# Performance work log

Measured on AMD Instinct MI355X. Metric: run time of the kernel, lower is better.

## Reference

```python
import jax, jax.numpy as jnp
import numpy as np

B, N, T, H = 128, 64, 1000, 16
TAU, VTH, EPS = 2.0, 0.5, 1e-5

# Heaviside spike with ATan surrogate gradient (alpha=2.0)
@jax.custom_vjp
def spike(u):
    return (u > 0).astype(u.dtype)

def _spike_fwd(u):
    return (u > 0).astype(u.dtype), u

def _spike_bwd(u, g):
    return (g / (1.0 + (2.0 * u) ** 2),)

spike.defvjp(_spike_fwd, _spike_bwd)


def setup_inputs() -> dict:
    key = jax.random.key(0)
    ks = jax.random.split(key, 6)
    x = jax.random.normal(ks[0], (B, 1, N, T), dtype=jnp.float32)
    # 1x1 Conv1d on a single input channel == per-output-channel scale + bias
    q_w = jax.random.normal(ks[1], (H,), dtype=jnp.float32) * 0.5
    q_b = jnp.zeros((H,), jnp.float32)
    k_w = jax.random.normal(ks[2], (H,), dtype=jnp.float32) * 0.5
    k_b = jnp.zeros((H,), jnp.float32)
    conv_w = jax.random.normal(ks[3], (H, 1, 1, 15), dtype=jnp.float32) * 0.1
    conv_b = jnp.zeros((H,), jnp.float32)
    bn_gamma = jnp.ones((H,), jnp.float32)
    bn_beta = jnp.zeros((H,), jnp.float32)
    fc_w = jax.random.normal(ks[4], (4, H * N), dtype=jnp.float32) * 0.02
    fc_b = jnp.zeros((4,), jnp.float32)
    return dict(x=x, q_w=q_w, q_b=q_b, k_w=k_w, k_b=k_b, conv_w=conv_w,
                conv_b=conv_b, bn_gamma=bn_gamma, bn_beta=bn_beta,
                fc_w=fc_w, fc_b=fc_b)


def reference(x, q_w, q_b, k_w, k_b, conv_w, conv_b, bn_gamma, bn_beta, fc_w, fc_b):
    xs = x[:, 0]                                    # [B, N, T]
    # Dynamic graph attention on per-channel variance "energy"
    energy = jnp.var(xs, axis=-1, ddof=1)           # [B, N] (torch unbiased var)
    Q = energy[:, None, :] * q_w[None, :, None] + q_b[None, :, None]  # [B,H,N]
    K = energy[:, None, :] * k_w[None, :, None] + k_b[None, :, None]
    attn = jnp.einsum('bhi,bhj->bij', Q, K) * (H ** -0.5)             # [B,N,N]
    attn = jnp.where(jnp.eye(N, dtype=bool)[None], -1e9, attn)
    w = jax.nn.softmax(attn, axis=-1)
    z_gcn = jnp.einsum('bij,bjt->bit', w, xs)[:, None] + x            # [B,1,N,T]
    # ANN spatial block: Conv2d(1,16,(1,15),pad=(0,7)) + BN (batch stats) + ELU
    z = jax.lax.conv_general_dilated(
        z_gcn, conv_w, window_strides=(1, 1), padding=((0, 0), (7, 7)),
        dimension_numbers=('NCHW', 'OIHW', 'NCHW')) + conv_b[None, :, None, None]
    mu = jnp.mean(z, axis=(0, 2, 3), keepdims=True)
    var = jnp.var(z, axis=(0, 2, 3), keepdims=True)
    z = (z - mu) * jax.lax.rsqrt(var + EPS)
    z = z * bn_gamma[None, :, None, None] + bn_beta[None, :, None, None]
    z = jax.nn.elu(z)                               # [B,H,N,T]
    # LIF temporal scan
    def step(v, xt):
        v = v * (1.0 - 1.0 / TAU) + xt
        s = spike(v - VTH)
        return v - s * VTH, s
    xt_seq = jnp.moveaxis(z, -1, 0)                 # [T,B,H,N]
    _, spikes = jax.lax.scan(step, jnp.zeros(z.shape[:-1], z.dtype), xt_seq)
    firing_rate = jnp.mean(spikes, axis=0)          # [B,H,N]
    z_feat = firing_rate.reshape(firing_rate.shape[0], -1)  # [B, H*N]
    logits = z_feat @ fc_w.T + fc_b                 # [B,4] (dropout = eval identity)
    return logits, z_feat, w
```

## Files before the change

kernel.cpp:

```cpp
#include <hip/hip_runtime.h>

#define B_ 128
#define N_ 64
#define T_ 1000
#define H_ 16

typedef float v2f __attribute__((ext_vector_type(2)));

__device__ __forceinline__ v2f mkv2(float a, float b) { v2f t; t.x = a; t.y = b; return t; }

__global__ __launch_bounds__(256) void k_energy(const float* __restrict__ x, float* __restrict__ energy) {
    int row = blockIdx.x;
    const float* xr = x + (size_t)row * T_;
    float s = 0.f, s2 = 0.f;
    for (int t4 = threadIdx.x; t4 < 250; t4 += 256) {
        float4 v = ((const float4*)xr)[t4];
        s += v.x + v.y + v.z + v.w;
        s2 += v.x*v.x + v.y*v.y + v.z*v.z + v.w*v.w;
    }
    __shared__ float r1[256], r2[256];
    r1[threadIdx.x] = s; r2[threadIdx.x] = s2;
    __syncthreads();
    for (int off = 128; off > 0; off >>= 1) {
        if (threadIdx.x < off) {
            r1[threadIdx.x] += r1[threadIdx.x + off];
            r2[threadIdx.x] += r2[threadIdx.x + off];
        }
        __syncthreads();
    }
    if (threadIdx.x == 0) {
        float S = r1[0], S2 = r2[0];
        energy[row] = (S2 - S * S / (float)T_) / (float)(T_ - 1);
    }
}

#define ZTC 128
__global__ __launch_bounds__(256) void k_zgcn(const float* __restrict__ energy,
        const float* __restrict__ q_w, const float* __restrict__ q_b,
        const float* __restrict__ k_w, const float* __restrict__ k_b,
        const float* __restrict__ x, float* __restrict__ zg,
        float* __restrict__ wmat_out, double* __restrict__ stats) {
    int b = blockIdx.y;
    int t0 = blockIdx.x * ZTC;
    int tid = threadIdx.x;
    if (blockIdx.x == 0 && b == 0 && tid < 163) stats[tid] = 0.0;
    __shared__ __attribute__((aligned(16))) float wsh[64 * 64];
    __shared__ __attribute__((aligned(16))) float xs[64][ZTC];
    __shared__ float en[64];
    float (*red1)[4] = (float(*)[4])&xs[0][0];
    float (*red2)[4] = (float(*)[4])&xs[2][0];
    if (tid < 64) en[tid] = energy[b * 64 + tid];
    __syncthreads();
    float alpha = 0.f, beta = 0.f;
    #pragma unroll
    for (int hh = 0; hh < H_; ++hh) {
        alpha = fmaf(q_w[hh], k_w[hh], alpha);
        beta  = fmaf(q_b[hh], k_w[hh], beta);
    }
    int row = tid >> 2, q = tid & 3;
    float si = 0.25f * fmaf(alpha, en[row], beta);
    float vals[16];
    float m = -3.0e38f;
    #pragma unroll
    for (int k = 0; k < 16; ++k) {
        int j = q * 16 + k;
        float a = si * en[j];
        if (j == row) a = -3.0e38f;
        vals[k] = a;
        m = fmaxf(m, a);
    }
    red1[row][q] = m;
    __syncthreads();
    float m4 = fmaxf(fmaxf(red1[row][0], red1[row][1]), fmaxf(red1[row][2], red1[row][3]));
    float sum = 0.f;
    #pragma unroll
    for (int k = 0; k < 16; ++k) {
        float p = __expf(vals[k] - m4);
        vals[k] = p;
        sum += p;
    }
    red2[row][q] = sum;
    __syncthreads();
    float den = red2[row][0] + red2[row][1] + red2[row][2] + red2[row][3];
    float inv = 1.f / den;
    #pragma unroll
    for (int k = 0; k < 16; ++k) vals[k] *= inv;
    __syncthreads();
    #pragma unroll
    for (int k = 0; k < 16; ++k) wsh[row * 64 + q * 16 + k] = vals[k];
    if (blockIdx.x == 0) {
        float* wr = wmat_out + (size_t)b * 4096 + row * 64 + q * 16;
        ((float4*)wr)[0] = float4{vals[0],  vals[1],  vals[2],  vals[3]};
        ((float4*)wr)[1] = float4{vals[4],  vals[5],  vals[6],  vals[7]};
        ((float4*)wr)[2] = float4{vals[8],  vals[9],  vals[10], vals[11]};
        ((float4*)wr)[3] = float4{vals[12], vals[13], vals[14], vals[15]};
    }
    const float* xb = x + (size_t)b * 64 * T_;
    for (int i = tid; i < 2048; i += 256) {
        int jj = i >> 5;
        int c4 = i & 31;
        int tt = t0 + c4 * 4;
        float4 val;
        if (tt + 3 < T_) val = *(const float4*)(xb + jj * T_ + tt);
        else {
            val.x = (tt     < T_) ? xb[jj * T_ + tt]     : 0.f;
            val.y = (tt + 1 < T_) ? xb[jj * T_ + tt + 1] : 0.f;
            val.z = (tt + 2 < T_) ? xb[jj * T_ + tt + 2] : 0.f;
            val.w = (tt + 3 < T_) ? xb[jj * T_ + tt + 3] : 0.f;
        }
        *(float4*)&xs[jj][c4 * 4] = val;
    }
    __syncthreads();
    int gi = tid >> 5, gt = tid & 31;
    int ii0 = gi * 8, tt0 = gt * 4;
    float4 acc[8];
    #pragma unroll
    for (int r = 0; r < 8; ++r) acc[r] = float4{0.f, 0.f, 0.f, 0.f};
    for (int jj = 0; jj < 64; ++jj) {
        float4 xv = *(const float4*)&xs[jj][tt0];
        #pragma unroll
        for (int r = 0; r < 8; ++r) {
            float wv = wsh[(ii0 + r) * 64 + jj];
            acc[r].x += wv * xv.x; acc[r].y += wv * xv.y;
            acc[r].z += wv * xv.z; acc[r].w += wv * xv.w;
        }
    }
    int tt = t0 + tt0;
    #pragma unroll
    for (int r = 0; r < 8; ++r) {
        float4 res = *(const float4*)&xs[ii0 + r][tt0];
        acc[r].x += res.x; acc[r].y += res.y; acc[r].z += res.z; acc[r].w += res.w;
        float* dst = zg + (size_t)b * 64 * T_ + (size_t)(ii0 + r) * T_;
        if (tt + 3 < T_) {
            *(float4*)(dst + tt) = acc[r];
        } else {
            if (tt     < T_) dst[tt]     = acc[r].x;
            if (tt + 1 < T_) dst[tt + 1] = acc[r].y;
            if (tt + 2 < T_) dst[tt + 2] = acc[r].z;
            if (tt + 3 < T_) dst[tt + 3] = acc[r].w;
        }
    }
}

__global__ __launch_bounds__(256) void k_autocorr(const float* __restrict__ zg, double* __restrict__ stats) {
    __shared__ float rows[8][1070];
    int row0 = blockIdx.x * 8;
    for (int idx = threadIdx.x; idx < 8 * 1070; idx += 256) {
        int rr = idx / 1070, j = idx - rr * 1070;
        rows[rr][j] = (j < T_) ? zg[(size_t)(row0 + rr) * T_ + j] : 0.f;
    }
    __syncthreads();
    int r = threadIdx.x >> 5, q = threadIdx.x & 31;
    const float* p = &rows[r][0];
    int t = q * 33;
    float w0=p[t+0], w1=p[t+1], w2=p[t+2], w3=p[t+3], w4=p[t+4], w5=p[t+5], w6=p[t+6],
          w7=p[t+7], w8=p[t+8], w9=p[t+9], w10=p[t+10], w11=p[t+11], w12=p[t+12], w13=p[t+13], w14;
    float a0=0.f,a1=0.f,a2=0.f,a3=0.f,a4=0.f,a5=0.f,a6=0.f,a7=0.f,a8=0.f,a9=0.f,
          a10=0.f,a11=0.f,a12=0.f,a13=0.f,a14=0.f, s1=0.f;
    #define ASTEP(wA,wB,wC,wD,wE,wF,wG,wH,wI,wJ,wK,wL,wM,wN,wO, off) { \
        wO = p[t + (off) + 14]; \
        s1 += wA; \
        a0  = fmaf(wA,wA,a0);  a1  = fmaf(wA,wB,a1);  a2  = fmaf(wA,wC,a2);  \
        a3  = fmaf(wA,wD,a3);  a4  = fmaf(wA,wE,a4);  a5  = fmaf(wA,wF,a5);  \
        a6  = fmaf(wA,wG,a6);  a7  = fmaf(wA,wH,a7);  a8  = fmaf(wA,wI,a8);  \
        a9  = fmaf(wA,wJ,a9);  a10 = fmaf(wA,wK,a10); a11 = fmaf(wA,wL,a11); \
        a12 = fmaf(wA,wM,a12); a13 = fmaf(wA,wN,a13); a14 = fmaf(wA,wO,a14); }
    #define AR0(o)  ASTEP(w0,w1,w2,w3,w4,w5,w6,w7,w8,w9,w10,w11,w12,w13,w14, o)
    #define AR1(o)  ASTEP(w1,w2,w3,w4,w5,w6,w7,w8,w9,w10,w11,w12,w13,w14,w0, o)
    #define AR2(o)  ASTEP(w2,w3,w4,w5,w6,w7,w8,w9,w10,w11,w12,w13,w14,w0,w1, o)
    #define AR3(o)  ASTEP(w3,w4,w5,w6,w7,w8,w9,w10,w11,w12,w13,w14,w0,w1,w2, o)
    #define AR4(o)  ASTEP(w4,w5,w6,w7,w8,w9,w10,w11,w12,w13,w14,w0,w1,w2,w3, o)
    #define AR5(o)  ASTEP(w5,w6,w7,w8,w9,w10,w11,w12,w13,w14,w0,w1,w2,w3,w4, o)
    #define AR6(o)  ASTEP(w6,w7,w8,w9,w10,w11,w12,w13,w14,w0,w1,w2,w3,w4,w5, o)
    #define AR7(o)  ASTEP(w7,w8,w9,w10,w11,w12,w13,w14,w0,w1,w2,w3,w4,w5,w6, o)
    #define AR8(o)  ASTEP(w8,w9,w10,w11,w12,w13,w14,w0,w1,w2,w3,w4,w5,w6,w7, o)
    #define AR9(o)  ASTEP(w9,w10,w11,w12,w13,w14,w0,w1,w2,w3,w4,w5,w6,w7,w8, o)
    #define AR10(o) ASTEP(w10,w11,w12,w13,w14,w0,w1,w2,w3,w4,w5,w6,w7,w8,w9, o)
    #define AR11(o) ASTEP(w11,w12,w13,w14,w0,w1,w2,w3,w4,w5,w6,w7,w8,w9,w10, o)
    #define AR12(o) ASTEP(w12,w13,w14,w0,w1,w2,w3,w4,w5,w6,w7,w8,w9,w10,w11, o)
    #define AR13(o) ASTEP(w13,w14,w0,w1,w2,w3,w4,w5,w6,w7,w8,w9,w10,w11,w12, o)
    #define AR14(o) ASTEP(w14,w0,w1,w2,w3,w4,w5,w6,w7,w8,w9,w10,w11,w12,w13, o)
    for (int mi = 0; mi < 2; ++mi) {
        AR0(0) AR1(1) AR2(2) AR3(3) AR4(4) AR5(5) AR6(6) AR7(7)
        AR8(8) AR9(9) AR10(10) AR11(11) AR12(12) AR13(13) AR14(14)
        t += 15;
    }
    AR0(0) AR1(1) AR2(2)
    #undef ASTEP
    __syncthreads();
    float eacc = 0.f;
    int v = threadIdx.x;
    if (v < 147) {
        int mode, ia, ib;
        if (v < 105) { mode = 0; ia = v / 15; ib = ia + (v % 15); }
        else if (v < 133) {
            int idx = v - 105; int i = 0, len = 7;
            while (idx >= len) { idx -= len; ++i; --len; }
            mode = 2; ia = 993 + i; ib = 993 + i + idx;
        }
        else if (v < 140) { mode = 1; ia = 0; ib = v - 133; }
        else { mode = 1; ia = 993 + (v - 140); ib = 999; }
        for (int rr = 0; rr < 8; ++rr) {
            const float* zr = &rows[rr][0];
            float val;
            if (mode != 1) val = zr[ia] * zr[ib];
            else { val = 0.f; for (int i = ia; i <= ib; ++i) val += zr[i]; }
            eacc += val;
        }
    }
    __syncthreads();
    float* red = &rows[0][0];
    int tid = threadIdx.x;
    red[tid*17+0]=a0;  red[tid*17+1]=a1;  red[tid*17+2]=a2;  red[tid*17+3]=a3;
    red[tid*17+4]=a4;  red[tid*17+5]=a5;  red[tid*17+6]=a6;  red[tid*17+7]=a7;
    red[tid*17+8]=a8;  red[tid*17+9]=a9;  red[tid*17+10]=a10; red[tid*17+11]=a11;
    red[tid*17+12]=a12; red[tid*17+13]=a13; red[tid*17+14]=a14; red[tid*17+15]=s1;
    __syncthreads();
    for (int off = 128; off > 0; off >>= 1) {
        if (tid < off)
            for (int k = 0; k < 16; ++k) red[tid*17+k] += red[(tid+off)*17+k];
        __syncthreads();
    }
    if (tid < 16) atomicAdd(&stats[tid], (double)red[tid]);
    if (v < 147) atomicAdd(&stats[16 + v], (double)eacc);
}

__global__ __launch_bounds__(256, 2) void k_scan(const float* __restrict__ zg,
        const double* __restrict__ stats, const float* __restrict__ conv_w,
        const float* __restrict__ gamma, const float* __restrict__ beta,
        float* __restrict__ zfeat) {
    int tid = threadIdx.x;
    int h = tid & 15, r = tid >> 4;
    int row0 = blockIdx.x * 16;
    __shared__ float scsh_s[256];
    if (tid < 16) {
        int hh = tid;
        const double M = (double)(B_ * N_) * (double)T_;
        double w[15];
        #pragma unroll
        for (int k = 0; k < 15; ++k) w[k] = (double)conv_w[hh * 15 + k];
        double SA = stats[15];
        const double* HP  = stats + 16;
        const double* TP  = stats + 16 + 105;
        const double* PRE = stats + 16 + 133;
        const double* SUF = stats + 16 + 140;
        double so = 0.0;
        #pragma unroll
        for (int k = 0; k < 15; ++k) {
            double U = SA;
            if (k < 7)      U -= SUF[k];
            else if (k > 7) U -= PRE[k - 8];
            so += w[k] * U;
        }
        double mean_o = so / M;
        double q = 0.0;
        #pragma unroll
        for (int k = 0; k < 15; ++k)
        #pragma unroll
        for (int k2 = 0; k2 < 15; ++k2) {
            int a = (k < k2) ? k : k2;
            int d = (k < k2) ? (k2 - k) : (k - k2);
            double G = stats[d];
            if (a >= 8)
                for (int i = 0; i <= a - 8; ++i) G -= HP[i * 15 + d];
            if (a + d <= 6)
                for (int i = a + 993; i <= 999 - d; ++i) {
                    int ip = i - 993;
                    G -= TP[ip * 7 - ip * (ip - 1) / 2 + d];
                }
            q += w[k] * w[k2] * G;
        }
        double var = q / M - mean_o * mean_o;
        double sc = (double)gamma[hh] / sqrt(var + 1e-5);
        scsh_s[240 + hh] = (float)((double)beta[hh] - mean_o * sc);
        #pragma unroll
        for (int k = 0; k < 15; ++k) scsh_s[hh * 15 + k] = (float)(w[k] * sc);
    }
    __syncthreads();
    float c0 = scsh_s[h*15+0],  c1 = scsh_s[h*15+1],  c2 = scsh_s[h*15+2],  c3 = scsh_s[h*15+3];
    float c4 = scsh_s[h*15+4],  c5 = scsh_s[h*15+5],  c6 = scsh_s[h*15+6],  c7 = scsh_s[h*15+7];
    float c8 = scsh_s[h*15+8],  c9 = scsh_s[h*15+9],  c10 = scsh_s[h*15+10], c11 = scsh_s[h*15+11];
    float c12 = scsh_s[h*15+12], c13 = scsh_s[h*15+13], c14 = scsh_s[h*15+14];
    float sh = scsh_s[240 + h];
    v2f d0 = {c0,c0},  d1 = {c1,c1},  d2 = {c2,c2},  d3 = {c3,c3},  d4 = {c4,c4};
    v2f d5 = {c5,c5},  d6 = {c6,c6},  d7 = {c7,c7},  d8 = {c8,c8},  d9 = {c9,c9};
    v2f d10 = {c10,c10}, d11 = {c11,c11}, d12 = {c12,c12}, d13 = {c13,c13}, d14 = {c14,c14};
    v2f shp2 = {sh, sh}, zr2 = {0.f, 0.f};
    const float* zrow = zg + (size_t)(row0 + r) * T_;
    float u = 2.f, cnt = 0.f;
    float4 g[17];
    const float4 f4z = {0.f, 0.f, 0.f, 0.f};

    #define PKF(acc, c, xp)  asm("v_pk_fma_f32 %0, %1, %2, %0" : "+v"(acc) : "v"(c), "v"(xp))
    #define PKADD(dd, aa, bb) asm("v_pk_add_f32 %0, %1, %2" : "=v"(dd) : "v"(aa), "v"(bb))

    #define PL(n) ( (((n)&3)==0) ? mkv2(g[(n)>>2].x, g[(n)>>2].y) \
                  : (((n)&3)==1) ? mkv2(g[(n)>>2].y, g[(n)>>2].z) \
                  : (((n)&3)==2) ? mkv2(g[(n)>>2].z, g[(n)>>2].w) \
                  :                mkv2(g[(n)>>2].w, g[((n)>>2)+1].x) )

    #define PAIRM(m) { \
        v2f vA = shp2, vB = zr2; \
        PKF(vA, d0,  PL(2*(m)+1));  PKF(vB, d1,  PL(2*(m)+2)); \
        PKF(vA, d2,  PL(2*(m)+3));  PKF(vB, d3,  PL(2*(m)+4)); \
        PKF(vA, d4,  PL(2*(m)+5));  PKF(vB, d5,  PL(2*(m)+6)); \
        PKF(vA, d6,  PL(2*(m)+7));  PKF(vB, d7,  PL(2*(m)+8)); \
        PKF(vA, d8,  PL(2*(m)+9));  PKF(vB, d9,  PL(2*(m)+10)); \
        PKF(vA, d10, PL(2*(m)+11)); PKF(vB, d11, PL(2*(m)+12)); \
        PKF(vA, d12, PL(2*(m)+13)); PKF(vB, d13, PL(2*(m)+14)); \
        PKF(vA, d14, PL(2*(m)+15)); \
        v2f vz; PKADD(vz, vA, vB); \
        float ex_ = __expf(fminf(vz.x, 0.f)); \
        float ey_ = __expf(fminf(vz.y, 0.f)); \
        float px_ = fmaxf(vz.x, 0.f) + ex_; \
        float py_ = fmaxf(vz.y, 0.f) + ey_; \
        u = fmaf(0.5f, u, px_); \
        float s0_ = (u > 2.5f) ? 1.f : 0.f; cnt += s0_; u = fmaf(-0.5f, s0_, u); \
        u = fmaf(0.5f, u, py_); \
        float s1_ = (u > 2.5f) ? 1.f : 0.f; cnt += s1_; u = fmaf(-0.5f, s1_, u); }

    #define PAIRS24 \
        PAIRM(0)  PAIRM(1)  PAIRM(2)  PAIRM(3)  PAIRM(4)  PAIRM(5) \
        PAIRM(6)  PAIRM(7)  PAIRM(8)  PAIRM(9)  PAIRM(10) PAIRM(11) \
        PAIRM(12) PAIRM(13) PAIRM(14) PAIRM(15) PAIRM(16) PAIRM(17) \
        PAIRM(18) PAIRM(19) PAIRM(20) PAIRM(21) PAIRM(22) PAIRM(23)

    #define PAIRS20 \
        PAIRM(0)  PAIRM(1)  PAIRM(2)  PAIRM(3)  PAIRM(4)  PAIRM(5) \
        PAIRM(6)  PAIRM(7)  PAIRM(8)  PAIRM(9)  PAIRM(10) PAIRM(11) \
        PAIRM(12) PAIRM(13) PAIRM(14) PAIRM(15) PAIRM(16) PAIRM(17) \
        PAIRM(18) PAIRM(19)

    {
        g[0] = f4z; g[1] = f4z;
        #pragma unroll
        for (int i = 2; i < 16; ++i) g[i] = *(const float4*)(zrow + 4*i - 8);
        PAIRS24
    }
    #pragma unroll 1
    for (int c = 1; c < 20; ++c) {
        const float* pc = zrow + 48*c - 8;
        #pragma unroll
        for (int i = 0; i < 16; ++i) g[i] = *(const float4*)(pc + 4*i);
        PAIRS24
    }
    {
        const float* pc = zrow + 952;
        #pragma unroll
        for (int i = 0; i < 12; ++i) g[i] = *(const float4*)(pc + 4*i);
        g[12] = f4z; g[13] = f4z; g[14] = f4z; g[15] = f4z;
        PAIRS20
    }
    #undef PKF
    #undef PKADD
    #undef PL
    #undef PAIRM
    #undef PAIRS24
    #undef PAIRS20
    int row = row0 + r;
    int b = row >> 6, i = row & 63;
    zfeat[(size_t)b * 1024 + h * 64 + i] = cnt * (1.0f / (float)T_);
}

__global__ __launch_bounds__(256) void k_fc(const float* __restrict__ zfeat, const float* __restrict__ fc_w,
                     const float* __restrict__ fc_b, float* __restrict__ logits) {
    int b = blockIdx.x;
    const float* zf = zfeat + (size_t)b * 1024;
    float a0 = 0.f, a1 = 0.f, a2 = 0.f, a3 = 0.f;
    for (int f = threadIdx.x; f < 1024; f += 256) {
        float z = zf[f];
        a0 += z * fc_w[f];
        a1 += z * fc_w[1024 + f];
        a2 += z * fc_w[2048 + f];
        a3 += z * fc_w[3072 + f];
    }
    __shared__ float red[4][256];
    red[0][threadIdx.x] = a0; red[1][threadIdx.x] = a1;
    red[2][threadIdx.x] = a2; red[3][threadIdx.x] = a3;
    __syncthreads();
    for (int off = 128; off > 0; off >>= 1) {
        if (threadIdx.x < off) {
            red[0][threadIdx.x] += red[0][threadIdx.x + off];
            red[1][threadIdx.x] += red[1][threadIdx.x + off];
            red[2][threadIdx.x] += red[2][threadIdx.x + off];
            red[3][threadIdx.x] += red[3][threadIdx.x + off];
        }
        __syncthreads();
    }
    if (threadIdx.x < 4) logits[b * 4 + threadIdx.x] = red[threadIdx.x][0] + fc_b[threadIdx.x];
}

extern "C" void kernel_launch(void* const* d_in, const int* in_sizes, int n_in,
                              void* d_out, int out_size, void* d_ws, size_t ws_size,
                              hipStream_t stream) {
    (void)in_sizes; (void)n_in; (void)out_size; (void)ws_size;
    const float* x      = (const float*)d_in[0];
    const float* q_w    = (const float*)d_in[1];
    const float* q_b    = (const float*)d_in[2];
    const float* k_w    = (const float*)d_in[3];
    const float* k_b    = (const float*)d_in[4];
    const float* conv_w = (const float*)d_in[5];
    const float* bn_g   = (const float*)d_in[7];
    const float* bn_b   = (const float*)d_in[8];
    const float* fc_w   = (const float*)d_in[9];
    const float* fc_b   = (const float*)d_in[10];

    float* out    = (float*)d_out;
    float* logits = out;
    float* zfeat  = out + 512;
    float* wmat   = out + 512 + 131072;

    char* ws      = (char*)d_ws;
    float* energy = (float*)ws;
    float* zg     = (float*)(ws + 32768);
    double* stats = (double*)(ws + 32768 + 32768000);

    k_energy<<<B_ * N_, 256, 0, stream>>>(x, energy);
    k_zgcn<<<dim3(8, B_), 256, 0, stream>>>(energy, q_w, q_b, k_w, k_b, x, zg, wmat, stats);
    k_autocorr<<<B_ * N_ / 8, 256, 0, stream>>>(zg, stats);
    k_scan<<<B_ * N_ / 16, 256, 0, stream>>>(zg, stats, conv_w, bn_g, bn_b, zfeat);
    k_fc<<<B_, 256, 0, stream>>>(zfeat, fc_w, fc_b, logits);
}
```

Baseline: 182.9 us.

## Stage scan input rows through double-buffered LDS with shifted copies for pair loads

The LIF scan kernel used to have each thread load its own overlapping float4 windows of its input row from global memory, so all 16 threads sharing a row loaded the same data. It now loads each 48-sample chunk of 16 rows cooperatively into a double-buffered LDS tile, plus a second copy shifted by one element so odd-offset pairs can be read as aligned 8-byte loads. The next chunk is prefetched into registers while the current one is computed, and a rotating register window reuses the pairs across steps. This cuts redundant global traffic and register pressure, and drops the occupancy hint from launch bounds, at the cost of LDS traffic and a barrier per chunk.

```diff
diff --git a/kernel.cpp b/kernel.cpp
--- a/kernel.cpp
+++ b/kernel.cpp
@@ -6,8 +6,6 @@
 #define H_ 16
 
 typedef float v2f __attribute__((ext_vector_type(2)));
-
-__device__ __forceinline__ v2f mkv2(float a, float b) { v2f t; t.x = a; t.y = b; return t; }
 
 __global__ __launch_bounds__(256) void k_energy(const float* __restrict__ x, float* __restrict__ energy) {
     int row = blockIdx.x;
@@ -225,14 +223,16 @@
     if (v < 147) atomicAdd(&stats[16 + v], (double)eacc);
 }
 
-__global__ __launch_bounds__(256, 2) void k_scan(const float* __restrict__ zg,
+__global__ __launch_bounds__(256) void k_scan(const float* __restrict__ zg,
         const double* __restrict__ stats, const float* __restrict__ conv_w,
         const float* __restrict__ gamma, const float* __restrict__ beta,
         float* __restrict__ zfeat) {
+    __shared__ float in_s[2][16][68];
+    __shared__ float in2[2][16][70];
+    __shared__ float scsh_s[256];
     int tid = threadIdx.x;
     int h = tid & 15, r = tid >> 4;
     int row0 = blockIdx.x * 16;
-    __shared__ float scsh_s[256];
     if (tid < 16) {
         int hh = tid;
         const double M = (double)(B_ * N_) * (double)T_;
@@ -286,77 +286,115 @@
     v2f d5 = {c5,c5},  d6 = {c6,c6},  d7 = {c7,c7},  d8 = {c8,c8},  d9 = {c9,c9};
     v2f d10 = {c10,c10}, d11 = {c11,c11}, d12 = {c12,c12}, d13 = {c13,c13}, d14 = {c14,c14};
     v2f shp2 = {sh, sh}, zr2 = {0.f, 0.f};
-    const float* zrow = zg + (size_t)(row0 + r) * T_;
     float u = 2.f, cnt = 0.f;
-    float4 g[17];
-    const float4 f4z = {0.f, 0.f, 0.f, 0.f};
-
-    #define PKF(acc, c, xp)  asm("v_pk_fma_f32 %0, %1, %2, %0" : "+v"(acc) : "v"(c), "v"(xp))
+    float ld0, ld1, ld2, ld3;
+    int su = tid & 63, sr = tid >> 6;
+
+    #define STAGE_LOAD(cc) { \
+        int g = (cc) * 48 - 8 + su; \
+        bool ok = (g >= 0 && g < T_); \
+        const float* zp_ = zg + (size_t)(row0 + sr) * T_ + g; \
+        ld0 = ok ? zp_[0] : 0.f; \
+        ld1 = ok ? zp_[4 * T_] : 0.f; \
+        ld2 = ok ? zp_[8 * T_] : 0.f; \
+        ld3 = ok ? zp_[12 * T_] : 0.f; }
+
+    #define STAGE_WRITE(db) { \
+        in_s[db][sr][su]       = ld0;  in2[db][sr][su + 1]       = ld0; \
+        in_s[db][sr + 4][su]   = ld1;  in2[db][sr + 4][su + 1]   = ld1; \
+        in_s[db][sr + 8][su]   = ld2;  in2[db][sr + 8][su + 1]   = ld2; \
+        in_s[db][sr + 12][su]  = ld3;  in2[db][sr + 12][su + 1]  = ld3; }
+
+    #define PKF(acc, cc, xp)  asm("v_pk_fma_f32 %0, %1, %2, %0" : "+v"(acc) : "v"(cc), "v"(xp))
     #define PKADD(dd, aa, bb) asm("v_pk_add_f32 %0, %1, %2" : "=v"(dd) : "v"(aa), "v"(bb))
 
-    #define PL(n) ( (((n)&3)==0) ? mkv2(g[(n)>>2].x, g[(n)>>2].y) \
-                  : (((n)&3)==1) ? mkv2(g[(n)>>2].y, g[(n)>>2].z) \
-                  : (((n)&3)==2) ? mkv2(g[(n)>>2].z, g[(n)>>2].w) \
-                  :                mkv2(g[(n)>>2].w, g[((n)>>2)+1].x) )
-
-    #define PAIRM(m) { \
+    #define EP(n) (*(const v2f*)(p2 + (n) + 1))
+    #define OP(n) (*(const v2f*)(pN + (n)))
+
+    #define PSTEP(Ea,Eb,Ec,Ed,Ee,Ef,Eg,Eh, Oa,Ob,Oc,Od,Oe,Of,Og, mm) { \
+        Eh = EP(2*(mm)+15); Og = OP(2*(mm)+14); \
         v2f vA = shp2, vB = zr2; \
-        PKF(vA, d0,  PL(2*(m)+1));  PKF(vB, d1,  PL(2*(m)+2)); \
-        PKF(vA, d2,  PL(2*(m)+3));  PKF(vB, d3,  PL(2*(m)+4)); \
-        PKF(vA, d4,  PL(2*(m)+5));  PKF(vB, d5,  PL(2*(m)+6)); \
-        PKF(vA, d6,  PL(2*(m)+7));  PKF(vB, d7,  PL(2*(m)+8)); \
-        PKF(vA, d8,  PL(2*(m)+9));  PKF(vB, d9,  PL(2*(m)+10)); \
-        PKF(vA, d10, PL(2*(m)+11)); PKF(vB, d11, PL(2*(m)+12)); \
-        PKF(vA, d12, PL(2*(m)+13)); PKF(vB, d13, PL(2*(m)+14)); \
-        PKF(vA, d14, PL(2*(m)+15)); \
+        PKF(vA, d0,  Ea); PKF(vB, d1,  Oa); \
+        PKF(vA, d2,  Eb); PKF(vB, d3,  Ob); \
+        PKF(vA, d4,  Ec); PKF(vB, d5,  Oc); \
+        PKF(vA, d6,  Ed); PKF(vB, d7,  Od); \
+        PKF(vA, d8,  Ee); PKF(vB, d9,  Oe); \
+        PKF(vA, d10, Ef); PKF(vB, d11, Of); \
+        PKF(vA, d12, Eg); PKF(vB, d13, Og); \
+        PKF(vA, d14, Eh); \
         v2f vz; PKADD(vz, vA, vB); \
-        float ex_ = __expf(fminf(vz.x, 0.f)); \
-        float ey_ = __expf(fminf(vz.y, 0.f)); \
-        float px_ = fmaxf(vz.x, 0.f) + ex_; \
-        float py_ = fmaxf(vz.y, 0.f) + ey_; \
-        u = fmaf(0.5f, u, px_); \
-        float s0_ = (u > 2.5f) ? 1.f : 0.f; cnt += s0_; u = fmaf(-0.5f, s0_, u); \
-        u = fmaf(0.5f, u, py_); \
-        float s1_ = (u > 2.5f) ? 1.f : 0.f; cnt += s1_; u = fmaf(-0.5f, s1_, u); }
-
-    #define PAIRS24 \
-        PAIRM(0)  PAIRM(1)  PAIRM(2)  PAIRM(3)  PAIRM(4)  PAIRM(5) \
-        PAIRM(6)  PAIRM(7)  PAIRM(8)  PAIRM(9)  PAIRM(10) PAIRM(11) \
-        PAIRM(12) PAIRM(13) PAIRM(14) PAIRM(15) PAIRM(16) PAIRM(17) \
-        PAIRM(18) PAIRM(19) PAIRM(20) PAIRM(21) PAIRM(22) PAIRM(23)
-
-    #define PAIRS20 \
-        PAIRM(0)  PAIRM(1)  PAIRM(2)  PAIRM(3)  PAIRM(4)  PAIRM(5) \
-        PAIRM(6)  PAIRM(7)  PAIRM(8)  PAIRM(9)  PAIRM(10) PAIRM(11) \
-        PAIRM(12) PAIRM(13) PAIRM(14) PAIRM(15) PAIRM(16) PAIRM(17) \
-        PAIRM(18) PAIRM(19)
-
+        float pe0 = fmaxf(vz.x, 0.f) + __expf(fminf(vz.x, 0.f)); \
+        u = fmaf(0.5f, u, pe0); \
+        float sp0 = (u > 2.5f) ? 1.f : 0.f; cnt += sp0; u = fmaf(-0.5f, sp0, u); \
+        float pe1 = fmaxf(vz.y, 0.f) + __expf(fminf(vz.y, 0.f)); \
+        u = fmaf(0.5f, u, pe1); \
+        float sp1 = (u > 2.5f) ? 1.f : 0.f; cnt += sp1; u = fmaf(-0.5f, sp1, u); }
+
+    #define PRELOAD \
+        v2f E0=EP(1), E1=EP(3), E2=EP(5), E3=EP(7), E4=EP(9), E5=EP(11), E6=EP(13), E7; \
+        v2f O0=OP(2), O1=OP(4), O2=OP(6), O3=OP(8), O4=OP(10), O5=OP(12), O6;
+
+    #define PS20 \
+        PSTEP(E0,E1,E2,E3,E4,E5,E6,E7, O0,O1,O2,O3,O4,O5,O6, 0) \
+        PSTEP(E1,E2,E3,E4,E5,E6,E7,E0, O1,O2,O3,O4,O5,O6,O0, 1) \
+        PSTEP(E2,E3,E4,E5,E6,E7,E0,E1, O2,O3,O4,O5,O6,O0,O1, 2) \
+        PSTEP(E3,E4,E5,E6,E7,E0,E1,E2, O3,O4,O5,O6,O0,O1,O2, 3) \
+        PSTEP(E4,E5,E6,E7,E0,E1,E2,E3, O4,O5,O6,O0,O1,O2,O3, 4) \
+        PSTEP(E5,E6,E7,E0,E1,E2,E3,E4, O5,O6,O0,O1,O2,O3,O4, 5) \
+        PSTEP(E6,E7,E0,E1,E2,E3,E4,E5, O6,O0,O1,O2,O3,O4,O5, 6) \
+        PSTEP(E7,E0,E1,E2,E3,E4,E5,E6, O0,O1,O2,O3,O4,O5,O6, 7) \
+        PSTEP(E0,E1,E2,E3,E4,E5,E6,E7, O1,O2,O3,O4,O5,O6,O0, 8) \
+        PSTEP(E1,E2,E3,E4,E5,E6,E7,E0, O2,O3,O4,O5,O6,O0,O1, 9) \
+        PSTEP(E2,E3,E4,E5,E6,E7,E0,E1, O3,O4,O5,O6,O0,O1,O2, 10) \
+        PSTEP(E3,E4,E5,E6,E7,E0,E1,E2, O4,O5,O6,O0,O1,O2,O3, 11) \
+        PSTEP(E4,E5,E6,E7,E0,E1,E2,E3, O5,O6,O0,O1,O2,O3,O4, 12) \
+        PSTEP(E5,E6,E7,E0,E1,E2,E3,E4, O6,O0,O1,O2,O3,O4,O5, 13) \
+        PSTEP(E6,E7,E0,E1,E2,E3,E4,E5, O0,O1,O2,O3,O4,O5,O6, 14) \
+        PSTEP(E7,E0,E1,E2,E3,E4,E5,E6, O1,O2,O3,O4,O5,O6,O0, 15) \
+        PSTEP(E0,E1,E2,E3,E4,E5,E6,E7, O2,O3,O4,O5,O6,O0,O1, 16) \
+        PSTEP(E1,E2,E3,E4,E5,E6,E7,E0, O3,O4,O5,O6,O0,O1,O2, 17) \
+        PSTEP(E2,E3,E4,E5,E6,E7,E0,E1, O4,O5,O6,O0,O1,O2,O3, 18) \
+        PSTEP(E3,E4,E5,E6,E7,E0,E1,E2, O5,O6,O0,O1,O2,O3,O4, 19)
+
+    #define PS24 PS20 \
+        PSTEP(E4,E5,E6,E7,E0,E1,E2,E3, O6,O0,O1,O2,O3,O4,O5, 20) \
+        PSTEP(E5,E6,E7,E0,E1,E2,E3,E4, O0,O1,O2,O3,O4,O5,O6, 21) \
+        PSTEP(E6,E7,E0,E1,E2,E3,E4,E5, O1,O2,O3,O4,O5,O6,O0, 22) \
+        PSTEP(E7,E0,E1,E2,E3,E4,E5,E6, O2,O3,O4,O5,O6,O0,O1, 23)
+
+    STAGE_LOAD(0)
+    STAGE_WRITE(0)
+    __syncthreads();
+    int buf = 0;
+    #pragma unroll 1
+    for (int c = 0; c < 20; ++c) {
+        STAGE_LOAD(c + 1)
+        {
+            const float* pN = &in_s[buf][r][0];
+            const float* p2 = &in2[buf][r][0];
+            PRELOAD
+            PS24
+        }
+        STAGE_WRITE(buf ^ 1)
+        __syncthreads();
+        buf ^= 1;
+    }
     {
-        g[0] = f4z; g[1] = f4z;
-        #pragma unroll
-        for (int i = 2; i < 16; ++i) g[i] = *(const float4*)(zrow + 4*i - 8);
-        PAIRS24
-    }
-    #pragma unroll 1
-    for (int c = 1; c < 20; ++c) {
-        const float* pc = zrow + 48*c - 8;
-        #pragma unroll
-        for (int i = 0; i < 16; ++i) g[i] = *(const float4*)(pc + 4*i);
-        PAIRS24
-    }
-    {
-        const float* pc = zrow + 952;
-        #pragma unroll
-        for (int i = 0; i < 12; ++i) g[i] = *(const float4*)(pc + 4*i);
-        g[12] = f4z; g[13] = f4z; g[14] = f4z; g[15] = f4z;
-        PAIRS20
-    }
+        const float* pN = &in_s[buf][r][0];
+        const float* p2 = &in2[buf][r][0];
+        PRELOAD
+        PS20
+    }
+    #undef STAGE_LOAD
+    #undef STAGE_WRITE
     #undef PKF
     #undef PKADD
-    #undef PL
-    #undef PAIRM
-    #undef PAIRS24
-    #undef PAIRS20
+    #undef EP
+    #undef OP
+    #undef PSTEP
+    #undef PRELOAD
+    #undef PS20
+    #undef PS24
     int row = row0 + r;
     int b = row >> 6, i = row & 63;
     zfeat[(size_t)b * 1024 + h * 64 + i] = cnt * (1.0f / (float)T_);
```

After: 182.4 us. No clear change (-0.3%).
